# Kernel tuning notes

Hardware: AMD Instinct MI355X
Metric: run time of the kernel (lower is better)

The kernel has to match this reference:

```python
import jax, jax.numpy as jnp
import numpy as np

EPS = 1e-5
B, S, P = 2, 512, 4096
TD, SD, H, ED = 512, 384, 8, 32
HD = TD // H


def _ln(x, g, b):
    m = jnp.mean(x, axis=-1, keepdims=True)
    v = jnp.var(x, axis=-1, keepdims=True)
    return (x - m) * jax.lax.rsqrt(v + EPS) * g + b


def setup_inputs() -> dict:
    key = jax.random.key(0)
    ks = iter(jax.random.split(key, 24))

    def lin(din, dout):
        W = jax.random.normal(next(ks), (din, dout), jnp.float32) / np.sqrt(din)
        b = jnp.zeros((dout,), jnp.float32)
        return W, b

    Wq, bq = lin(TD, TD)
    Wk, bk = lin(SD, TD)
    Wv, bv = lin(SD, TD)
    Wo, bo = lin(TD, TD)
    W1, b1 = lin(TD, 4 * TD)
    W2, b2 = lin(4 * TD, TD)
    edge_emb = jax.random.normal(next(ks), (H, ED), jnp.float32)
    ep_w = jax.random.normal(next(ks), (ED,), jnp.float32) / np.sqrt(ED)
    ep_b = jnp.zeros((), jnp.float32)

    return dict(
        text_features=jax.random.normal(next(ks), (B, S, TD), jnp.float32),
        shape_features=jax.random.normal(next(ks), (B, P, SD), jnp.float32),
        tn_g=jnp.ones((TD,), jnp.float32), tn_b=jnp.zeros((TD,), jnp.float32),
        sn_g=jnp.ones((SD,), jnp.float32), sn_b=jnp.zeros((SD,), jnp.float32),
        Wq=Wq, bq=bq, Wk=Wk, bk=bk, Wv=Wv, bv=bv,
        edge_emb=edge_emb, ep_w=ep_w, ep_b=ep_b,
        Wo=Wo, bo=bo,
        on_g=jnp.ones((TD,), jnp.float32), on_b=jnp.zeros((TD,), jnp.float32),
        W1=W1, b1=b1, W2=W2, b2=b2,
        fn_g=jnp.ones((TD,), jnp.float32), fn_b=jnp.zeros((TD,), jnp.float32),
    )


def reference(text_features, shape_features, tn_g, tn_b, sn_g, sn_b,
              Wq, bq, Wk, bk, Wv, bv, edge_emb, ep_w, ep_b, Wo, bo,
              on_g, on_b, W1, b1, W2, b2, fn_g, fn_b):
    b, n, _ = text_features.shape
    tn = _ln(text_features, tn_g, tn_b)
    sn = _ln(shape_features, sn_g, sn_b)
    residual = text_features

    # [b, h, n, d] projections
    q = (tn @ Wq + bq).reshape(b, n, H, HD).transpose(0, 2, 1, 3)
    k = (sn @ Wk + bk).reshape(b, -1, H, HD).transpose(0, 2, 1, 3)
    v = (sn @ Wv + bv).reshape(b, -1, H, HD).transpose(0, 2, 1, 3)

    scale = HD ** -0.5
    base_attn = jnp.einsum('bhid,bhjd->bhij', q, k) * scale  # [b,h,n,p]

    # edge_attn[:,h] = base_attn[:,h,:,:,None] * edge_emb[h]; then Linear(ED,1)+LeakyReLU.
    # Algebraically: score = leaky_relu(base_attn * (edge_emb @ ep_w) + ep_b)
    s = edge_emb @ ep_w  # [H] per-head scalar
    edge_scores = jax.nn.leaky_relu(base_attn * s[None, :, None, None] + ep_b, 0.2)

    attn = jax.nn.softmax(base_attn + edge_scores, axis=-1)
    out = jnp.einsum('bhij,bhjd->bhid', attn, v)
    out = out.transpose(0, 2, 1, 3).reshape(b, n, TD)
    out = out @ Wo + bo
    out = _ln(residual + out, on_g, on_b)

    ffn = jax.nn.gelu(out @ W1 + b1, approximate=False) @ W2 + b2
    out = _ln(out + ffn, fn_g, fn_b)
    return out, attn
```

## Files before the change

### kernel.cpp

```cpp
#include <hip/hip_runtime.h>
#include <math.h>

#define B_  2
#define S_  512
#define P_  4096
#define TD_ 512
#define SD_ 384
#define H_  8
#define HD_ 64
#define FF_ 2048

typedef _Float16 half8 __attribute__((ext_vector_type(8)));
typedef _Float16 half4 __attribute__((ext_vector_type(4)));
typedef float floatx4 __attribute__((ext_vector_type(4)));

__device__ __forceinline__ float2 block_sum2(float a, float b) {
    for (int off = 32; off > 0; off >>= 1) {
        a += __shfl_down(a, off);
        b += __shfl_down(b, off);
    }
    __shared__ float sa[8], sb[8];
    int w = threadIdx.x >> 6;
    if ((threadIdx.x & 63) == 0) { sa[w] = a; sb[w] = b; }
    __syncthreads();
    int nw = blockDim.x >> 6;
    float ta = 0.f, tb = 0.f;
    for (int i = 0; i < nw; ++i) { ta += sa[i]; tb += sb[i]; }
    __syncthreads();
    return make_float2(ta, tb);
}

__global__ __launch_bounds__(256) void prep_kernel(
    const float* __restrict__ s0p, const float* __restrict__ s1p,
    const float* __restrict__ s2p, const float* __restrict__ s3p,
    const float* __restrict__ s4p, const float* __restrict__ s5p,
    _Float16* __restrict__ d0p, _Float16* __restrict__ d1p,
    _Float16* __restrict__ d2p, _Float16* __restrict__ d3p,
    _Float16* __restrict__ d4p, _Float16* __restrict__ d5p,
    const float* __restrict__ text, const float* __restrict__ shape,
    const float* __restrict__ tn_g, const float* __restrict__ tn_b,
    const float* __restrict__ sn_g, const float* __restrict__ sn_b,
    _Float16* __restrict__ tn_h, _Float16* __restrict__ sn_h)
{
    __shared__ float ts[32][33];
    int id = blockIdx.x;
    int tid = threadIdx.x;
    if (id < 2944) {
        const float* src; _Float16* dst; int K, N, t, nlog;
        if (id < 256)       { src=s0p; dst=d0p; K=512;  N=512;  t=id;       nlog=4; }
        else if (id < 448)  { src=s1p; dst=d1p; K=384;  N=512;  t=id-256;   nlog=4; }
        else if (id < 640)  { src=s2p; dst=d2p; K=384;  N=512;  t=id-448;   nlog=4; }
        else if (id < 896)  { src=s3p; dst=d3p; K=512;  N=512;  t=id-640;   nlog=4; }
        else if (id < 1920) { src=s4p; dst=d4p; K=512;  N=2048; t=id-896;   nlog=6; }
        else                { src=s5p; dst=d5p; K=2048; N=512;  t=id-1920;  nlog=4; }
        int n0 = (t & ((1 << nlog) - 1)) << 5;
        int k0 = (t >> nlog) << 5;
#pragma unroll
        for (int i = 0; i < 4; ++i) {
            int e = i * 256 + tid;
            int kk = e >> 5, nn = e & 31;
            ts[kk][nn] = src[(size_t)(k0 + kk) * N + n0 + nn];
        }
        __syncthreads();
#pragma unroll
        for (int i = 0; i < 4; ++i) {
            int e = i * 256 + tid;
            int nn = e >> 5, kk = e & 31;
            dst[(size_t)(n0 + nn) * K + k0 + kk] = (_Float16)ts[kk][nn];
        }
        return;
    }
    int row = id - 2944;
    const float* xr; const float* g; const float* be; _Float16* yr; int D;
    if (row < 1024) {
        D = 512; xr = text + (size_t)row * 512; g = tn_g; be = tn_b;
        yr = tn_h + (size_t)row * 512;
    } else {
        int r2 = row - 1024;
        D = 384; xr = shape + (size_t)r2 * 384; g = sn_g; be = sn_b;
        yr = sn_h + (size_t)r2 * 384;
    }
    float s = 0.f, s2 = 0.f;
    for (int i = tid; i < D; i += 256) {
        float v = xr[i]; s += v; s2 += v * v;
    }
    float2 r = block_sum2(s, s2);
    float mean = r.x / (float)D;
    float var  = r.y / (float)D - mean * mean;
    float rstd = rsqrtf(var + 1e-5f);
    for (int i = tid; i < D; i += 256)
        yr[i] = (_Float16)((xr[i] - mean) * rstd * g[i] + be[i]);
}

__global__ __launch_bounds__(256) void ln_add_kernel(
    const float* __restrict__ a, const float* __restrict__ c, int np, int cstride,
    const float* __restrict__ g, const float* __restrict__ be,
    float* __restrict__ yf, _Float16* __restrict__ yh)
{
    int row = blockIdx.x;
    int i0 = threadIdx.x, i1 = threadIdx.x + 256;
    const float* ar = a + (size_t)row * 512;
    const float* cr = c + (size_t)row * 512;
    float v0 = ar[i0], v1 = ar[i1];
    for (int t = 0; t < np; ++t) {
        v0 += cr[(size_t)t * cstride + i0];
        v1 += cr[(size_t)t * cstride + i1];
    }
    float2 rd = block_sum2(v0 + v1, v0 * v0 + v1 * v1);
    float mean = rd.x / 512.f;
    float var  = rd.y / 512.f - mean * mean;
    float rstd = rsqrtf(var + 1e-5f);
    float o0 = (v0 - mean) * rstd * g[i0] + be[i0];
    float o1 = (v1 - mean) * rstd * g[i1] + be[i1];
    if (yf) { yf[(size_t)row * 512 + i0] = o0; yf[(size_t)row * 512 + i1] = o1; }
    if (yh) { yh[(size_t)row * 512 + i0] = (_Float16)o0; yh[(size_t)row * 512 + i1] = (_Float16)o1; }
}

template<int ACT, int OUTF, int OUTH, int SPLITK>
__global__ __launch_bounds__(256) void gemm_f16_kernel(
    const _Float16* __restrict__ A, const _Float16* __restrict__ Bt,
    const float* __restrict__ bias, float* __restrict__ Cf,
    _Float16* __restrict__ Ch, int M, int N, int K)
{
    __shared__ _Float16 As[128 * 40];
    __shared__ _Float16 Bs[128 * 40];
    int tid = threadIdx.x;
    int bm = blockIdx.y * 128, bn = blockIdx.x * 128;
    int wave = tid >> 6, lane = tid & 63, quad = lane >> 4, r = lane & 15;
    int mh = (wave & 1) * 64, nh = (wave >> 1) * 64;

    floatx4 acc[4][4];
    floatx4 zz = {0.f, 0.f, 0.f, 0.f};
#pragma unroll
    for (int i = 0; i < 4; ++i)
#pragma unroll
        for (int j = 0; j < 4; ++j) acc[i][j] = zz;

    int srow = tid >> 2;
    int sko  = (tid & 3) * 8;

    int ksplit = (SPLITK > 1) ? blockIdx.z : 0;
    int kbeg = ksplit * (K / SPLITK);
    int kend = kbeg + K / SPLITK;

    const _Float16* Ap0 = A  + (size_t)(bm + srow) * K + sko;
    const _Float16* Ap1 = A  + (size_t)(bm + srow + 64) * K + sko;
    const _Float16* Bp0 = Bt + (size_t)(bn + srow) * K + sko;
    const _Float16* Bp1 = Bt + (size_t)(bn + srow + 64) * K + sko;

    half8 ra0 = *(const half8*)(Ap0 + kbeg);
    half8 ra1 = *(const half8*)(Ap1 + kbeg);
    half8 rb0 = *(const half8*)(Bp0 + kbeg);
    half8 rb1 = *(const half8*)(Bp1 + kbeg);

    for (int k0 = kbeg; k0 < kend; k0 += 32) {
        *(half8*)&As[srow * 40 + sko]        = ra0;
        *(half8*)&As[(srow + 64) * 40 + sko] = ra1;
        *(half8*)&Bs[srow * 40 + sko]        = rb0;
        *(half8*)&Bs[(srow + 64) * 40 + sko] = rb1;
        __syncthreads();
        if (k0 + 32 < kend) {
            ra0 = *(const half8*)(Ap0 + k0 + 32);
            ra1 = *(const half8*)(Ap1 + k0 + 32);
            rb0 = *(const half8*)(Bp0 + k0 + 32);
            rb1 = *(const half8*)(Bp1 + k0 + 32);
        }
        half8 af[4], bf[4];
#pragma unroll
        for (int t = 0; t < 4; ++t) {
            af[t] = *(const half8*)&As[(mh + t * 16 + r) * 40 + quad * 8];
            bf[t] = *(const half8*)&Bs[(nh + t * 16 + r) * 40 + quad * 8];
        }
#pragma unroll
        for (int i = 0; i < 4; ++i)
#pragma unroll
            for (int j = 0; j < 4; ++j)
                acc[i][j] = __builtin_amdgcn_mfma_f32_16x16x32_f16(af[i], bf[j], acc[i][j], 0, 0, 0);
        __syncthreads();
    }

#pragma unroll
    for (int j = 0; j < 4; ++j) {
        int col = bn + nh + j * 16 + r;
        float bv = (SPLITK == 1 || ksplit == 0) ? bias[col] : 0.f;
#pragma unroll
        for (int i = 0; i < 4; ++i) {
#pragma unroll
            for (int g = 0; g < 4; ++g) {
                int row = bm + mh + i * 16 + quad * 4 + g;
                float v = acc[i][j][g] + bv;
                if (ACT) v = 0.5f * v * (1.0f + erff(v * 0.70710678118654752f));
                if (OUTF) Cf[(size_t)ksplit * M * N + (size_t)row * N + col] = v;
                if (OUTH) Ch[(size_t)row * N + col] = (_Float16)v;
            }
        }
    }
}

__global__ __launch_bounds__(256) void qkv_gemm_kernel(
    const _Float16* __restrict__ tn, const _Float16* __restrict__ sn,
    const _Float16* __restrict__ Wqt, const _Float16* __restrict__ Wkt,
    const _Float16* __restrict__ Wvt,
    const float* __restrict__ bq, const float* __restrict__ bk,
    const float* __restrict__ bv,
    _Float16* __restrict__ Qh, _Float16* __restrict__ Kh, _Float16* __restrict__ Vth)
{
    __shared__ _Float16 As[128 * 40];
    __shared__ _Float16 Bs[128 * 40];
    int by = blockIdx.y;
    const _Float16* A; const _Float16* Bt; const float* bias; _Float16* out;
    int K, bm, vt;
    if (by < 8)       { A = tn; Bt = Wqt; bias = bq; K = 512; bm = by * 128;        vt = 0; out = Qh;  }
    else if (by < 72) { A = sn; Bt = Wkt; bias = bk; K = 384; bm = (by - 8) * 128;  vt = 0; out = Kh;  }
    else              { A = sn; Bt = Wvt; bias = bv; K = 384; bm = (by - 72) * 128; vt = 1; out = Vth; }
    int bn = blockIdx.x * 128;
    int tid = threadIdx.x;
    int wave = tid >> 6, lane = tid & 63, quad = lane >> 4, r = lane & 15;
    int mh = (wave & 1) * 64, nh = (wave >> 1) * 64;

    floatx4 acc[4][4];
    floatx4 zz = {0.f, 0.f, 0.f, 0.f};
#pragma unroll
    for (int i = 0; i < 4; ++i)
#pragma unroll
        for (int j = 0; j < 4; ++j) acc[i][j] = zz;

    int srow = tid >> 2;
    int sko  = (tid & 3) * 8;

    const _Float16* Ap0 = A  + (size_t)(bm + srow) * K + sko;
    const _Float16* Ap1 = A  + (size_t)(bm + srow + 64) * K + sko;
    const _Float16* Bp0 = Bt + (size_t)(bn + srow) * K + sko;
    const _Float16* Bp1 = Bt + (size_t)(bn + srow + 64) * K + sko;

    half8 ra0 = *(const half8*)(Ap0);
    half8 ra1 = *(const half8*)(Ap1);
    half8 rb0 = *(const half8*)(Bp0);
    half8 rb1 = *(const half8*)(Bp1);

    for (int k0 = 0; k0 < K; k0 += 32) {
        *(half8*)&As[srow * 40 + sko]        = ra0;
        *(half8*)&As[(srow + 64) * 40 + sko] = ra1;
        *(half8*)&Bs[srow * 40 + sko]        = rb0;
        *(half8*)&Bs[(srow + 64) * 40 + sko] = rb1;
        __syncthreads();
        if (k0 + 32 < K) {
            ra0 = *(const half8*)(Ap0 + k0 + 32);
            ra1 = *(const half8*)(Ap1 + k0 + 32);
            rb0 = *(const half8*)(Bp0 + k0 + 32);
            rb1 = *(const half8*)(Bp1 + k0 + 32);
        }
        half8 af[4], bf[4];
#pragma unroll
        for (int t = 0; t < 4; ++t) {
            af[t] = *(const half8*)&As[(mh + t * 16 + r) * 40 + quad * 8];
            bf[t] = *(const half8*)&Bs[(nh + t * 16 + r) * 40 + quad * 8];
        }
#pragma unroll
        for (int i = 0; i < 4; ++i)
#pragma unroll
            for (int j = 0; j < 4; ++j)
                acc[i][j] = __builtin_amdgcn_mfma_f32_16x16x32_f16(af[i], bf[j], acc[i][j], 0, 0, 0);
        __syncthreads();
    }

#pragma unroll
    for (int j = 0; j < 4; ++j) {
        int col = bn + nh + j * 16 + r;
        float bvv = bias[col];
#pragma unroll
        for (int i = 0; i < 4; ++i) {
#pragma unroll
            for (int g = 0; g < 4; ++g) {
                int row = bm + mh + i * 16 + quad * 4 + g;
                float v = acc[i][j][g] + bvv;
                if (!vt) {
                    out[(size_t)row * 512 + col] = (_Float16)v;
                } else {
                    int bb = row >> 12, pp = row & 4095;
                    int hh = col >> 6,  dd = col & 63;
                    out[((size_t)((bb * 8 + hh) * 64 + dd)) * 4096 + pp] = (_Float16)v;
                }
            }
        }
    }
}

__global__ __launch_bounds__(256) void score_stats_kernel(
    const _Float16* __restrict__ Qh, const _Float16* __restrict__ Kh,
    const float* __restrict__ edge_emb, const float* __restrict__ ep_w,
    const float* __restrict__ ep_b, float2* __restrict__ part)
{
    __shared__ _Float16 Qs[128 * 72];
    __shared__ _Float16 Ks[128 * 72];
    __shared__ float mred[2][128];
    __shared__ float sred[2][128];
    int p0 = blockIdx.x * 128, s0 = blockIdx.y * 128;
    int bh = blockIdx.z, h = bh & 7, b = bh >> 3;
    int tid = threadIdx.x;
    int wave = tid >> 6, lane = tid & 63, quad = lane >> 4, r = lane & 15;
    int mh = (wave & 1) * 64, nh = (wave >> 1) * 64;

#pragma unroll
    for (int i = 0; i < 4; ++i) {
        int row = i * 32 + (tid >> 3);
        int ko  = (tid & 7) * 8;
        *(half8*)&Qs[row * 72 + ko] = *(const half8*)(Qh + (size_t)(b * S_ + s0 + row) * TD_ + h * HD_ + ko);
        *(half8*)&Ks[row * 72 + ko] = *(const half8*)(Kh + (size_t)(b * P_ + p0 + row) * TD_ + h * HD_ + ko);
    }
    float s_h = 0.f;
#pragma unroll
    for (int e = 0; e < 32; ++e) s_h += edge_emb[h * 32 + e] * ep_w[e];
    float epbv = ep_b[0];
    __syncthreads();

    floatx4 acc[4][4];
    floatx4 zz = {0.f, 0.f, 0.f, 0.f};
#pragma unroll
    for (int i = 0; i < 4; ++i)
#pragma unroll
        for (int j = 0; j < 4; ++j) acc[i][j] = zz;

#pragma unroll
    for (int c = 0; c < 2; ++c) {
        half8 af[4], bf[4];
#pragma unroll
        for (int t = 0; t < 4; ++t) {
            af[t] = *(const half8*)&Qs[(mh + t * 16 + r) * 72 + c * 32 + quad * 8];
            bf[t] = *(const half8*)&Ks[(nh + t * 16 + r) * 72 + c * 32 + quad * 8];
        }
#pragma unroll
        for (int i = 0; i < 4; ++i)
#pragma unroll
            for (int j = 0; j < 4; ++j)
                acc[i][j] = __builtin_amdgcn_mfma_f32_16x16x32_f16(af[i], bf[j], acc[i][j], 0, 0, 0);
    }

    const float scale = 0.125f;
#pragma unroll
    for (int i = 0; i < 4; ++i)
#pragma unroll
        for (int j = 0; j < 4; ++j)
#pragma unroll
            for (int g = 0; g < 4; ++g) {
                float base = acc[i][j][g] * scale;
                float t = fmaf(base, s_h, epbv);
                float e = (t >= 0.f) ? t : 0.2f * t;
                acc[i][j][g] = base + e;
            }

    float mv[16], sv[16];
#pragma unroll
    for (int i = 0; i < 4; ++i)
#pragma unroll
        for (int g = 0; g < 4; ++g)
            mv[i * 4 + g] = fmaxf(fmaxf(acc[i][0][g], acc[i][1][g]),
                                  fmaxf(acc[i][2][g], acc[i][3][g]));
#pragma unroll
    for (int mask = 1; mask <= 8; mask <<= 1)
#pragma unroll
        for (int t = 0; t < 16; ++t)
            mv[t] = fmaxf(mv[t], __shfl_xor(mv[t], mask));
#pragma unroll
    for (int i = 0; i < 4; ++i)
#pragma unroll
        for (int g = 0; g < 4; ++g) {
            float s = 0.f;
#pragma unroll
            for (int j = 0; j < 4; ++j) s += __expf(acc[i][j][g] - mv[i * 4 + g]);
            sv[i * 4 + g] = s;
        }
#pragma unroll
    for (int mask = 1; mask <= 8; mask <<= 1)
#pragma unroll
        for (int t = 0; t < 16; ++t)
            sv[t] += __shfl_xor(sv[t], mask);

    if (r == 0) {
#pragma unroll
        for (int i = 0; i < 4; ++i)
#pragma unroll
            for (int g = 0; g < 4; ++g) {
                int row = mh + i * 16 + quad * 4 + g;
                mred[wave >> 1][row] = mv[i * 4 + g];
                sred[wave >> 1][row] = sv[i * 4 + g];
            }
    }
    __syncthreads();
    if (tid < 128) {
        float m0 = mred[0][tid], m1 = mred[1][tid];
        float m = fmaxf(m0, m1);
        float s = sred[0][tid] * __expf(m0 - m) + sred[1][tid] * __expf(m1 - m);
        part[(size_t)blockIdx.x * (B_ * H_ * S_) + (size_t)bh * S_ + s0 + tid] = make_float2(m, s);
    }
}

__global__ __launch_bounds__(256) void attn_pv_kernel(
    const _Float16* __restrict__ Qh, const _Float16* __restrict__ Kh,
    const _Float16* __restrict__ Vt,
    const float* __restrict__ edge_emb, const float* __restrict__ ep_w,
    const float* __restrict__ ep_b, const float2* __restrict__ part,
    float* __restrict__ attn, float* __restrict__ ctx_part)
{
    __shared__ _Float16 Qs[32 * 72];
    __shared__ _Float16 Ks[128 * 72];
    __shared__ _Float16 Vs[64 * 136];
    __shared__ _Float16 As[32 * 136];
    __shared__ float2 ms_sh[32];

    int s0 = blockIdx.x * 32;
    int split = blockIdx.y;
    int bh = blockIdx.z, h = bh & 7, b = bh >> 3;
    int tid = threadIdx.x;
    int wave = tid >> 6, lane = tid & 63, quad = lane >> 4, r = lane & 15;

    {
        int row = tid >> 3, ko = (tid & 7) * 8;
        *(half8*)&Qs[row * 72 + ko] =
            *(const half8*)(Qh + (size_t)(b * S_ + s0 + row) * TD_ + h * HD_ + ko);
    }
    if (tid < 32) {
        int base = bh * S_ + s0 + tid;
        float2 v = part[base];
        float m = v.x, l = v.y;
#pragma unroll
        for (int t = 1; t < 32; ++t) {
            float2 p = part[(size_t)t * (B_ * H_ * S_) + base];
            float nm = fmaxf(m, p.x);
            l = l * __expf(m - nm) + p.y * __expf(p.x - nm);
            m = nm;
        }
        ms_sh[tid] = make_float2(m, 1.0f / l);
    }

    float s_h = 0.f;
#pragma unroll
    for (int e = 0; e < 32; ++e) s_h += edge_emb[h * 32 + e] * ep_w[e];
    float epbv = ep_b[0];

    const _Float16* Kbase = Kh + (size_t)b * P_ * TD_ + h * HD_;
    const _Float16* Vbase = Vt + (size_t)bh * 64 * P_;

    int pg0 = split * 512;
    half8 rk[4], rv[4];
#pragma unroll
    for (int ii = 0; ii < 4; ++ii) {
        int e = ii * 256 + tid;
        rk[ii] = *(const half8*)(Kbase + (size_t)(pg0 + (e >> 3)) * TD_ + (e & 7) * 8);
        rv[ii] = *(const half8*)(Vbase + (size_t)(e >> 4) * P_ + pg0 + (e & 15) * 8);
    }

    floatx4 zz = {0.f, 0.f, 0.f, 0.f};
    floatx4 accpv[2];
    accpv[0] = zz; accpv[1] = zz;
    const float scale = 0.125f;

    for (int c = 0; c < 4; ++c) {
        int pg = pg0 + c * 128;
#pragma unroll
        for (int ii = 0; ii < 4; ++ii) {
            int e = ii * 256 + tid;
            *(half8*)&Ks[(e >> 3) * 72 + (e & 7) * 8]  = rk[ii];
            *(half8*)&Vs[(e >> 4) * 136 + (e & 15) * 8] = rv[ii];
        }
        __syncthreads();
        if (c < 3) {
            int pn = pg + 128;
#pragma unroll
            for (int ii = 0; ii < 4; ++ii) {
                int e = ii * 256 + tid;
                rk[ii] = *(const half8*)(Kbase + (size_t)(pn + (e >> 3)) * TD_ + (e & 7) * 8);
                rv[ii] = *(const half8*)(Vbase + (size_t)(e >> 4) * P_ + pn + (e & 15) * 8);
            }
        }

        floatx4 accs[2][2];
        accs[0][0] = zz; accs[0][1] = zz; accs[1][0] = zz; accs[1][1] = zz;
#pragma unroll
        for (int c2 = 0; c2 < 2; ++c2) {
            half8 aq[2], bk2[2];
#pragma unroll
            for (int i = 0; i < 2; ++i)
                aq[i] = *(const half8*)&Qs[(i * 16 + r) * 72 + c2 * 32 + quad * 8];
#pragma unroll
            for (int j = 0; j < 2; ++j)
                bk2[j] = *(const half8*)&Ks[(wave * 32 + j * 16 + r) * 72 + c2 * 32 + quad * 8];
#pragma unroll
            for (int i = 0; i < 2; ++i)
#pragma unroll
                for (int j = 0; j < 2; ++j)
                    accs[i][j] = __builtin_amdgcn_mfma_f32_16x16x32_f16(aq[i], bk2[j], accs[i][j], 0, 0, 0);
        }

#pragma unroll
        for (int i = 0; i < 2; ++i)
#pragma unroll
            for (int j = 0; j < 2; ++j) {
                int colp = wave * 32 + j * 16 + r;
#pragma unroll
                for (int g = 0; g < 4; ++g) {
                    int srow = i * 16 + quad * 4 + g;
                    float base = accs[i][j][g] * scale;
                    float t = fmaf(base, s_h, epbv);
                    float e = (t >= 0.f) ? t : 0.2f * t;
                    float z = base + e;
                    float2 ms = ms_sh[srow];
                    float p = __expf(z - ms.x) * ms.y;
                    __builtin_nontemporal_store(p, &attn[((size_t)bh * S_ + s0 + srow) * P_ + pg + colp]);
                    As[srow * 136 + colp] = (_Float16)p;
                }
            }
        __syncthreads();

#pragma unroll
        for (int cc = 0; cc < 4; ++cc) {
            half8 bv = *(const half8*)&Vs[(wave * 16 + r) * 136 + cc * 32 + quad * 8];
#pragma unroll
            for (int i2 = 0; i2 < 2; ++i2) {
                half8 ap = *(const half8*)&As[(i2 * 16 + r) * 136 + cc * 32 + quad * 8];
                accpv[i2] = __builtin_amdgcn_mfma_f32_16x16x32_f16(ap, bv, accpv[i2], 0, 0, 0);
            }
        }
        __syncthreads();
    }

    float* dst = ctx_part + (size_t)split * (1024 * 512);
#pragma unroll
    for (int i2 = 0; i2 < 2; ++i2)
#pragma unroll
        for (int g = 0; g < 4; ++g) {
            int srow = s0 + i2 * 16 + quad * 4 + g;
            int d = wave * 16 + r;
            dst[(size_t)(b * S_ + srow) * TD_ + h * HD_ + d] = accpv[i2][g];
        }
}

__global__ __launch_bounds__(256) void sumcast_kernel(
    const float4* __restrict__ src, _Float16* __restrict__ dst, int n4)
{
    int i = blockIdx.x * 256 + threadIdx.x;
    if (i < n4) {
        float4 v = src[i];
#pragma unroll
        for (int t = 1; t < 8; ++t) {
            float4 p = src[i + t * 131072];
            v.x += p.x; v.y += p.y; v.z += p.z; v.w += p.w;
        }
        half4 hv = { (_Float16)v.x, (_Float16)v.y, (_Float16)v.z, (_Float16)v.w };
        *(half4*)&dst[(size_t)i * 4] = hv;
    }
}

extern "C" void kernel_launch(void* const* d_in, const int* in_sizes, int n_in,
                              void* d_out, int out_size, void* d_ws, size_t ws_size,
                              hipStream_t stream) {
    const float* text  = (const float*)d_in[0];
    const float* shape = (const float*)d_in[1];
    const float* tn_g  = (const float*)d_in[2];
    const float* tn_b  = (const float*)d_in[3];
    const float* sn_g  = (const float*)d_in[4];
    const float* sn_b  = (const float*)d_in[5];
    const float* Wq    = (const float*)d_in[6];
    const float* bq    = (const float*)d_in[7];
    const float* Wk    = (const float*)d_in[8];
    const float* bk    = (const float*)d_in[9];
    const float* Wv    = (const float*)d_in[10];
    const float* bv    = (const float*)d_in[11];
    const float* edge  = (const float*)d_in[12];
    const float* epw   = (const float*)d_in[13];
    const float* epb   = (const float*)d_in[14];
    const float* Wo    = (const float*)d_in[15];
    const float* bo    = (const float*)d_in[16];
    const float* on_g  = (const float*)d_in[17];
    const float* on_b  = (const float*)d_in[18];
    const float* W1    = (const float*)d_in[19];
    const float* b1    = (const float*)d_in[20];
    const float* W2    = (const float*)d_in[21];
    const float* b2    = (const float*)d_in[22];
    const float* fn_g  = (const float*)d_in[23];
    const float* fn_b  = (const float*)d_in[24];

    float* out_f  = (float*)d_out;
    float* attn_f = out_f + (size_t)B_ * S_ * TD_;

    char* w = (char*)d_ws;
    _Float16* tn_h   = (_Float16*)w; w += (size_t)1024 * 512 * 2;
    _Float16* sn_h   = (_Float16*)w; w += (size_t)8192 * 384 * 2;
    _Float16* Q_h    = (_Float16*)w; w += (size_t)1024 * 512 * 2;
    _Float16* K_h    = (_Float16*)w; w += (size_t)8192 * 512 * 2;
    _Float16* Vt_h   = (_Float16*)w; w += (size_t)16 * 64 * 4096 * 2;
    _Float16* ctx_h  = (_Float16*)w; w += (size_t)1024 * 512 * 2;
    _Float16* out1_h = (_Float16*)w; w += (size_t)1024 * 512 * 2;
    _Float16* h1_h   = (_Float16*)w; w += (size_t)1024 * 2048 * 2;
    _Float16* Wqt    = (_Float16*)w; w += (size_t)512 * 512 * 2;
    _Float16* Wkt    = (_Float16*)w; w += (size_t)512 * 384 * 2;
    _Float16* Wvt    = (_Float16*)w; w += (size_t)512 * 384 * 2;
    _Float16* Wot    = (_Float16*)w; w += (size_t)512 * 512 * 2;
    _Float16* W1t    = (_Float16*)w; w += (size_t)2048 * 512 * 2;
    _Float16* W2t    = (_Float16*)w; w += (size_t)512 * 2048 * 2;
    float*    out1_f = (float*)w;    w += (size_t)1024 * 512 * 4;
    float*    ctx_part = (float*)w;  w += (size_t)8 * 1024 * 512 * 4;

    float2* part = (float2*)sn_h;

    prep_kernel<<<2944 + 1024 + 8192, 256, 0, stream>>>(
        Wq, Wk, Wv, Wo, W1, W2, Wqt, Wkt, Wvt, Wot, W1t, W2t,
        text, shape, tn_g, tn_b, sn_g, sn_b, tn_h, sn_h);

    qkv_gemm_kernel<<<dim3(4, 136), 256, 0, stream>>>(tn_h, sn_h, Wqt, Wkt, Wvt,
                                                      bq, bk, bv, Q_h, K_h, Vt_h);

    score_stats_kernel<<<dim3(P_ / 128, S_ / 128, B_ * H_), 256, 0, stream>>>(
        Q_h, K_h, edge, epw, epb, part);
    attn_pv_kernel<<<dim3(S_ / 32, 8, B_ * H_), 256, 0, stream>>>(
        Q_h, K_h, Vt_h, edge, epw, epb, part, attn_f, ctx_part);
    sumcast_kernel<<<dim3(512), 256, 0, stream>>>((const float4*)ctx_part, ctx_h, 131072);

    gemm_f16_kernel<0,1,0,4><<<dim3(4, 8, 4), 256, 0, stream>>>(ctx_h, Wot, bo, ctx_part, nullptr, 1024, 512, 512);
    ln_add_kernel<<<B_ * S_, 256, 0, stream>>>(text, ctx_part, 4, 1024 * 512, on_g, on_b, out1_f, out1_h);

    gemm_f16_kernel<1,0,1,1><<<dim3(16, 8), 256, 0, stream>>>(out1_h, W1t, b1, nullptr, h1_h, 1024, 2048, 512);
    gemm_f16_kernel<0,1,0,4><<<dim3(4, 8, 4), 256, 0, stream>>>(h1_h, W2t, b2, ctx_part, nullptr, 1024, 512, 2048);
    ln_add_kernel<<<B_ * S_, 256, 0, stream>>>(out1_f, ctx_part, 4, 1024 * 512, fn_g, fn_b, out_f, nullptr);
}
```

Before: 356.2 us.

## Fuse softmax stats and PV into single two-pass attention kernel; enlarge QKV tiles

Replaces the separate score-statistics kernel, the split-P attention/PV kernel and the ctx sum-cast kernel with one kernel per (32-query block, head). It makes two passes over all of P: the first builds the running max and sum, the second writes normalized probabilities and accumulates PV directly into fp16 ctx. This removes the partial-stat buffer, the 8-way ctx partials and the reduction kernel. In exchange the grid shrinks to 256 blocks that each loop over 4096 keys twice, which cuts parallelism and recomputes QK^T. The QKV GEMM also moves to 512-thread blocks with 256-row A tiles.

New measurement: 391.1 us. +9.8%, slower.

```diff
diff --git a/kernel.cpp b/kernel.cpp
--- a/kernel.cpp
+++ b/kernel.cpp
@@ -197,7 +197,7 @@
     }
 }
 
-__global__ __launch_bounds__(256) void qkv_gemm_kernel(
+__global__ __launch_bounds__(512) void qkv_gemm_kernel(
     const _Float16* __restrict__ tn, const _Float16* __restrict__ sn,
     const _Float16* __restrict__ Wqt, const _Float16* __restrict__ Wkt,
     const _Float16* __restrict__ Wvt,
@@ -205,18 +205,18 @@
     const float* __restrict__ bv,
     _Float16* __restrict__ Qh, _Float16* __restrict__ Kh, _Float16* __restrict__ Vth)
 {
-    __shared__ _Float16 As[128 * 40];
+    __shared__ _Float16 As[256 * 40];
     __shared__ _Float16 Bs[128 * 40];
     int by = blockIdx.y;
     const _Float16* A; const _Float16* Bt; const float* bias; _Float16* out;
     int K, bm, vt;
-    if (by < 8)       { A = tn; Bt = Wqt; bias = bq; K = 512; bm = by * 128;        vt = 0; out = Qh;  }
-    else if (by < 72) { A = sn; Bt = Wkt; bias = bk; K = 384; bm = (by - 8) * 128;  vt = 0; out = Kh;  }
-    else              { A = sn; Bt = Wvt; bias = bv; K = 384; bm = (by - 72) * 128; vt = 1; out = Vth; }
+    if (by < 4)       { A = tn; Bt = Wqt; bias = bq; K = 512; bm = by * 256;        vt = 0; out = Qh;  }
+    else if (by < 36) { A = sn; Bt = Wkt; bias = bk; K = 384; bm = (by - 4) * 256;  vt = 0; out = Kh;  }
+    else              { A = sn; Bt = Wvt; bias = bv; K = 384; bm = (by - 36) * 256; vt = 1; out = Vth; }
     int bn = blockIdx.x * 128;
     int tid = threadIdx.x;
     int wave = tid >> 6, lane = tid & 63, quad = lane >> 4, r = lane & 15;
-    int mh = (wave & 1) * 64, nh = (wave >> 1) * 64;
+    int mh = (wave >> 1) * 64, nh = (wave & 1) * 64;
 
     floatx4 acc[4][4];
     floatx4 zz = {0.f, 0.f, 0.f, 0.f};
@@ -225,30 +225,24 @@
 #pragma unroll
         for (int j = 0; j < 4; ++j) acc[i][j] = zz;
 
-    int srow = tid >> 2;
-    int sko  = (tid & 3) * 8;
-
-    const _Float16* Ap0 = A  + (size_t)(bm + srow) * K + sko;
-    const _Float16* Ap1 = A  + (size_t)(bm + srow + 64) * K + sko;
-    const _Float16* Bp0 = Bt + (size_t)(bn + srow) * K + sko;
-    const _Float16* Bp1 = Bt + (size_t)(bn + srow + 64) * K + sko;
-
-    half8 ra0 = *(const half8*)(Ap0);
-    half8 ra1 = *(const half8*)(Ap1);
-    half8 rb0 = *(const half8*)(Bp0);
-    half8 rb1 = *(const half8*)(Bp1);
+    int arow = tid >> 2, ako = (tid & 3) * 8;
+    const _Float16* ApA0 = A  + (size_t)(bm + arow) * K + ako;
+    const _Float16* ApA1 = A  + (size_t)(bm + arow + 128) * K + ako;
+    const _Float16* BpB  = Bt + (size_t)(bn + arow) * K + ako;
+
+    half8 ra0 = *(const half8*)(ApA0);
+    half8 ra1 = *(const half8*)(ApA1);
+    half8 rb  = *(const half8*)(BpB);
 
     for (int k0 = 0; k0 < K; k0 += 32) {
-        *(half8*)&As[srow * 40 + sko]        = ra0;
-        *(half8*)&As[(srow + 64) * 40 + sko] = ra1;
-        *(half8*)&Bs[srow * 40 + sko]        = rb0;
-        *(half8*)&Bs[(srow + 64) * 40 + sko] = rb1;
+        *(half8*)&As[arow * 40 + ako]         = ra0;
+        *(half8*)&As[(arow + 128) * 40 + ako] = ra1;
+        *(half8*)&Bs[arow * 40 + ako]         = rb;
         __syncthreads();
         if (k0 + 32 < K) {
-            ra0 = *(const half8*)(Ap0 + k0 + 32);
-            ra1 = *(const half8*)(Ap1 + k0 + 32);
-            rb0 = *(const half8*)(Bp0 + k0 + 32);
-            rb1 = *(const half8*)(Bp1 + k0 + 32);
+            ra0 = *(const half8*)(ApA0 + k0 + 32);
+            ra1 = *(const half8*)(ApA1 + k0 + 32);
+            rb  = *(const half8*)(BpB  + k0 + 32);
         }
         half8 af[4], bf[4];
 #pragma unroll
@@ -286,268 +280,176 @@
     }
 }
 
-__global__ __launch_bounds__(256) void score_stats_kernel(
-    const _Float16* __restrict__ Qh, const _Float16* __restrict__ Kh,
-    const float* __restrict__ edge_emb, const float* __restrict__ ep_w,
-    const float* __restrict__ ep_b, float2* __restrict__ part)
-{
-    __shared__ _Float16 Qs[128 * 72];
-    __shared__ _Float16 Ks[128 * 72];
-    __shared__ float mred[2][128];
-    __shared__ float sred[2][128];
-    int p0 = blockIdx.x * 128, s0 = blockIdx.y * 128;
-    int bh = blockIdx.z, h = bh & 7, b = bh >> 3;
-    int tid = threadIdx.x;
-    int wave = tid >> 6, lane = tid & 63, quad = lane >> 4, r = lane & 15;
-    int mh = (wave & 1) * 64, nh = (wave >> 1) * 64;
-
-#pragma unroll
-    for (int i = 0; i < 4; ++i) {
-        int row = i * 32 + (tid >> 3);
-        int ko  = (tid & 7) * 8;
-        *(half8*)&Qs[row * 72 + ko] = *(const half8*)(Qh + (size_t)(b * S_ + s0 + row) * TD_ + h * HD_ + ko);
-        *(half8*)&Ks[row * 72 + ko] = *(const half8*)(Kh + (size_t)(b * P_ + p0 + row) * TD_ + h * HD_ + ko);
-    }
-    float s_h = 0.f;
-#pragma unroll
-    for (int e = 0; e < 32; ++e) s_h += edge_emb[h * 32 + e] * ep_w[e];
-    float epbv = ep_b[0];
-    __syncthreads();
-
-    floatx4 acc[4][4];
-    floatx4 zz = {0.f, 0.f, 0.f, 0.f};
-#pragma unroll
-    for (int i = 0; i < 4; ++i)
-#pragma unroll
-        for (int j = 0; j < 4; ++j) acc[i][j] = zz;
-
-#pragma unroll
-    for (int c = 0; c < 2; ++c) {
-        half8 af[4], bf[4];
-#pragma unroll
-        for (int t = 0; t < 4; ++t) {
-            af[t] = *(const half8*)&Qs[(mh + t * 16 + r) * 72 + c * 32 + quad * 8];
-            bf[t] = *(const half8*)&Ks[(nh + t * 16 + r) * 72 + c * 32 + quad * 8];
-        }
-#pragma unroll
-        for (int i = 0; i < 4; ++i)
-#pragma unroll
-            for (int j = 0; j < 4; ++j)
-                acc[i][j] = __builtin_amdgcn_mfma_f32_16x16x32_f16(af[i], bf[j], acc[i][j], 0, 0, 0);
-    }
-
-    const float scale = 0.125f;
-#pragma unroll
-    for (int i = 0; i < 4; ++i)
-#pragma unroll
-        for (int j = 0; j < 4; ++j)
-#pragma unroll
-            for (int g = 0; g < 4; ++g) {
-                float base = acc[i][j][g] * scale;
-                float t = fmaf(base, s_h, epbv);
-                float e = (t >= 0.f) ? t : 0.2f * t;
-                acc[i][j][g] = base + e;
-            }
-
-    float mv[16], sv[16];
-#pragma unroll
-    for (int i = 0; i < 4; ++i)
-#pragma unroll
-        for (int g = 0; g < 4; ++g)
-            mv[i * 4 + g] = fmaxf(fmaxf(acc[i][0][g], acc[i][1][g]),
-                                  fmaxf(acc[i][2][g], acc[i][3][g]));
-#pragma unroll
-    for (int mask = 1; mask <= 8; mask <<= 1)
-#pragma unroll
-        for (int t = 0; t < 16; ++t)
-            mv[t] = fmaxf(mv[t], __shfl_xor(mv[t], mask));
-#pragma unroll
-    for (int i = 0; i < 4; ++i)
-#pragma unroll
-        for (int g = 0; g < 4; ++g) {
-            float s = 0.f;
-#pragma unroll
-            for (int j = 0; j < 4; ++j) s += __expf(acc[i][j][g] - mv[i * 4 + g]);
-            sv[i * 4 + g] = s;
-        }
-#pragma unroll
-    for (int mask = 1; mask <= 8; mask <<= 1)
-#pragma unroll
-        for (int t = 0; t < 16; ++t)
-            sv[t] += __shfl_xor(sv[t], mask);
-
-    if (r == 0) {
-#pragma unroll
-        for (int i = 0; i < 4; ++i)
-#pragma unroll
-            for (int g = 0; g < 4; ++g) {
-                int row = mh + i * 16 + quad * 4 + g;
-                mred[wave >> 1][row] = mv[i * 4 + g];
-                sred[wave >> 1][row] = sv[i * 4 + g];
-            }
-    }
-    __syncthreads();
-    if (tid < 128) {
-        float m0 = mred[0][tid], m1 = mred[1][tid];
-        float m = fmaxf(m0, m1);
-        float s = sred[0][tid] * __expf(m0 - m) + sred[1][tid] * __expf(m1 - m);
-        part[(size_t)blockIdx.x * (B_ * H_ * S_) + (size_t)bh * S_ + s0 + tid] = make_float2(m, s);
-    }
-}
-
-__global__ __launch_bounds__(256) void attn_pv_kernel(
+__global__ __launch_bounds__(512) void flash_attn_kernel(
     const _Float16* __restrict__ Qh, const _Float16* __restrict__ Kh,
     const _Float16* __restrict__ Vt,
     const float* __restrict__ edge_emb, const float* __restrict__ ep_w,
-    const float* __restrict__ ep_b, const float2* __restrict__ part,
-    float* __restrict__ attn, float* __restrict__ ctx_part)
+    const float* __restrict__ ep_b,
+    float* __restrict__ attn, _Float16* __restrict__ ctx_h)
 {
     __shared__ _Float16 Qs[32 * 72];
     __shared__ _Float16 Ks[128 * 72];
     __shared__ _Float16 Vs[64 * 136];
     __shared__ _Float16 As[32 * 136];
-    __shared__ float2 ms_sh[32];
+    __shared__ float cm[8][32], cl[8][32];
 
     int s0 = blockIdx.x * 32;
-    int split = blockIdx.y;
-    int bh = blockIdx.z, h = bh & 7, b = bh >> 3;
+    int bh = blockIdx.y, h = bh & 7, b = bh >> 3;
     int tid = threadIdx.x;
     int wave = tid >> 6, lane = tid & 63, quad = lane >> 4, r = lane & 15;
-
-    {
+    int sH = wave >> 2, pQ = wave & 3;
+
+    if (tid < 256) {
         int row = tid >> 3, ko = (tid & 7) * 8;
         *(half8*)&Qs[row * 72 + ko] =
             *(const half8*)(Qh + (size_t)(b * S_ + s0 + row) * TD_ + h * HD_ + ko);
     }
-    if (tid < 32) {
-        int base = bh * S_ + s0 + tid;
-        float2 v = part[base];
-        float m = v.x, l = v.y;
-#pragma unroll
-        for (int t = 1; t < 32; ++t) {
-            float2 p = part[(size_t)t * (B_ * H_ * S_) + base];
-            float nm = fmaxf(m, p.x);
-            l = l * __expf(m - nm) + p.y * __expf(p.x - nm);
-            m = nm;
-        }
-        ms_sh[tid] = make_float2(m, 1.0f / l);
-    }
-
     float s_h = 0.f;
 #pragma unroll
     for (int e = 0; e < 32; ++e) s_h += edge_emb[h * 32 + e] * ep_w[e];
     float epbv = ep_b[0];
+    const float scale = 0.125f;
 
     const _Float16* Kbase = Kh + (size_t)b * P_ * TD_ + h * HD_;
     const _Float16* Vbase = Vt + (size_t)bh * 64 * P_;
 
-    int pg0 = split * 512;
-    half8 rk[4], rv[4];
-#pragma unroll
-    for (int ii = 0; ii < 4; ++ii) {
-        int e = ii * 256 + tid;
-        rk[ii] = *(const half8*)(Kbase + (size_t)(pg0 + (e >> 3)) * TD_ + (e & 7) * 8);
-        rv[ii] = *(const half8*)(Vbase + (size_t)(e >> 4) * P_ + pg0 + (e & 15) * 8);
-    }
+    int krow = tid >> 3, kko = (tid & 7) * 8;
+    int vrow = tid >> 4, vpo = (tid & 15) * 8;
 
     floatx4 zz = {0.f, 0.f, 0.f, 0.f};
-    floatx4 accpv[2];
-    accpv[0] = zz; accpv[1] = zz;
-    const float scale = 0.125f;
-
-    for (int c = 0; c < 4; ++c) {
-        int pg = pg0 + c * 128;
-#pragma unroll
-        for (int ii = 0; ii < 4; ++ii) {
-            int e = ii * 256 + tid;
-            *(half8*)&Ks[(e >> 3) * 72 + (e & 7) * 8]  = rk[ii];
-            *(half8*)&Vs[(e >> 4) * 136 + (e & 15) * 8] = rv[ii];
-        }
-        __syncthreads();
-        if (c < 3) {
-            int pn = pg + 128;
-#pragma unroll
-            for (int ii = 0; ii < 4; ++ii) {
-                int e = ii * 256 + tid;
-                rk[ii] = *(const half8*)(Kbase + (size_t)(pn + (e >> 3)) * TD_ + (e & 7) * 8);
-                rv[ii] = *(const half8*)(Vbase + (size_t)(e >> 4) * P_ + pn + (e & 15) * 8);
-            }
-        }
-
-        floatx4 accs[2][2];
-        accs[0][0] = zz; accs[0][1] = zz; accs[1][0] = zz; accs[1][1] = zz;
+    float m_run[4], l_run[4];
+#pragma unroll
+    for (int g = 0; g < 4; ++g) { m_run[g] = -1e30f; l_run[g] = 0.f; }
+
+    half8 rk0 = *(const half8*)(Kbase + (size_t)krow * TD_ + kko);
+    half8 rk1 = *(const half8*)(Kbase + (size_t)(krow + 64) * TD_ + kko);
+
+    for (int pc = 0; pc < P_; pc += 128) {
+        *(half8*)&Ks[krow * 72 + kko]        = rk0;
+        *(half8*)&Ks[(krow + 64) * 72 + kko] = rk1;
+        __syncthreads();
+        if (pc + 128 < P_) {
+            rk0 = *(const half8*)(Kbase + (size_t)(pc + 128 + krow) * TD_ + kko);
+            rk1 = *(const half8*)(Kbase + (size_t)(pc + 128 + krow + 64) * TD_ + kko);
+        }
+        floatx4 accs[2];
+        accs[0] = zz; accs[1] = zz;
 #pragma unroll
         for (int c2 = 0; c2 < 2; ++c2) {
-            half8 aq[2], bk2[2];
-#pragma unroll
-            for (int i = 0; i < 2; ++i)
-                aq[i] = *(const half8*)&Qs[(i * 16 + r) * 72 + c2 * 32 + quad * 8];
-#pragma unroll
-            for (int j = 0; j < 2; ++j)
-                bk2[j] = *(const half8*)&Ks[(wave * 32 + j * 16 + r) * 72 + c2 * 32 + quad * 8];
-#pragma unroll
-            for (int i = 0; i < 2; ++i)
-#pragma unroll
-                for (int j = 0; j < 2; ++j)
-                    accs[i][j] = __builtin_amdgcn_mfma_f32_16x16x32_f16(aq[i], bk2[j], accs[i][j], 0, 0, 0);
-        }
-
-#pragma unroll
-        for (int i = 0; i < 2; ++i)
+            half8 aq = *(const half8*)&Qs[(sH * 16 + r) * 72 + c2 * 32 + quad * 8];
 #pragma unroll
             for (int j = 0; j < 2; ++j) {
-                int colp = wave * 32 + j * 16 + r;
-#pragma unroll
-                for (int g = 0; g < 4; ++g) {
-                    int srow = i * 16 + quad * 4 + g;
-                    float base = accs[i][j][g] * scale;
-                    float t = fmaf(base, s_h, epbv);
-                    float e = (t >= 0.f) ? t : 0.2f * t;
-                    float z = base + e;
-                    float2 ms = ms_sh[srow];
-                    float p = __expf(z - ms.x) * ms.y;
-                    __builtin_nontemporal_store(p, &attn[((size_t)bh * S_ + s0 + srow) * P_ + pg + colp]);
-                    As[srow * 136 + colp] = (_Float16)p;
-                }
-            }
-        __syncthreads();
-
+                half8 bk = *(const half8*)&Ks[(pQ * 32 + j * 16 + r) * 72 + c2 * 32 + quad * 8];
+                accs[j] = __builtin_amdgcn_mfma_f32_16x16x32_f16(aq, bk, accs[j], 0, 0, 0);
+            }
+        }
+        float zv[2][4];
+#pragma unroll
+        for (int j = 0; j < 2; ++j)
+#pragma unroll
+            for (int g = 0; g < 4; ++g) {
+                float base = accs[j][g] * scale;
+                float t = fmaf(base, s_h, epbv);
+                float e = (t >= 0.f) ? t : 0.2f * t;
+                zv[j][g] = base + e;
+            }
+        float mw[4], sw[4];
+#pragma unroll
+        for (int g = 0; g < 4; ++g) {
+            mw[g] = fmaxf(zv[0][g], zv[1][g]);
+#pragma unroll
+            for (int mask = 1; mask <= 8; mask <<= 1)
+                mw[g] = fmaxf(mw[g], __shfl_xor(mw[g], mask));
+            sw[g] = __expf(zv[0][g] - mw[g]) + __expf(zv[1][g] - mw[g]);
+#pragma unroll
+            for (int mask = 1; mask <= 8; mask <<= 1)
+                sw[g] += __shfl_xor(sw[g], mask);
+        }
+        if (r == 0) {
+#pragma unroll
+            for (int g = 0; g < 4; ++g) {
+                cm[wave][sH * 16 + quad * 4 + g] = mw[g];
+                cl[wave][sH * 16 + quad * 4 + g] = sw[g];
+            }
+        }
+        __syncthreads();
+#pragma unroll
+        for (int g = 0; g < 4; ++g) {
+            int row = sH * 16 + quad * 4 + g;
+#pragma unroll
+            for (int q2 = 0; q2 < 4; ++q2) {
+                float mc = cm[sH * 4 + q2][row];
+                float lc = cl[sH * 4 + q2][row];
+                float nm = fmaxf(m_run[g], mc);
+                l_run[g] = l_run[g] * __expf(m_run[g] - nm) + lc * __expf(mc - nm);
+                m_run[g] = nm;
+            }
+        }
+    }
+    float invl[4];
+#pragma unroll
+    for (int g = 0; g < 4; ++g) invl[g] = 1.0f / l_run[g];
+
+    half8 prk0 = *(const half8*)(Kbase + (size_t)krow * TD_ + kko);
+    half8 prk1 = *(const half8*)(Kbase + (size_t)(krow + 64) * TD_ + kko);
+    half8 prv0 = *(const half8*)(Vbase + (size_t)vrow * P_ + vpo);
+    half8 prv1 = *(const half8*)(Vbase + (size_t)(vrow + 32) * P_ + vpo);
+
+    floatx4 accpv = zz;
+
+    for (int pc = 0; pc < P_; pc += 128) {
+        *(half8*)&Ks[krow * 72 + kko]         = prk0;
+        *(half8*)&Ks[(krow + 64) * 72 + kko]  = prk1;
+        *(half8*)&Vs[vrow * 136 + vpo]        = prv0;
+        *(half8*)&Vs[(vrow + 32) * 136 + vpo] = prv1;
+        __syncthreads();
+        if (pc + 128 < P_) {
+            prk0 = *(const half8*)(Kbase + (size_t)(pc + 128 + krow) * TD_ + kko);
+            prk1 = *(const half8*)(Kbase + (size_t)(pc + 128 + krow + 64) * TD_ + kko);
+            prv0 = *(const half8*)(Vbase + (size_t)vrow * P_ + pc + 128 + vpo);
+            prv1 = *(const half8*)(Vbase + (size_t)(vrow + 32) * P_ + pc + 128 + vpo);
+        }
+        floatx4 accs[2];
+        accs[0] = zz; accs[1] = zz;
+#pragma unroll
+        for (int c2 = 0; c2 < 2; ++c2) {
+            half8 aq = *(const half8*)&Qs[(sH * 16 + r) * 72 + c2 * 32 + quad * 8];
+#pragma unroll
+            for (int j = 0; j < 2; ++j) {
+                half8 bk = *(const half8*)&Ks[(pQ * 32 + j * 16 + r) * 72 + c2 * 32 + quad * 8];
+                accs[j] = __builtin_amdgcn_mfma_f32_16x16x32_f16(aq, bk, accs[j], 0, 0, 0);
+            }
+        }
+#pragma unroll
+        for (int j = 0; j < 2; ++j) {
+            int colp = pQ * 32 + j * 16 + r;
+#pragma unroll
+            for (int g = 0; g < 4; ++g) {
+                int srow = sH * 16 + quad * 4 + g;
+                float base = accs[j][g] * scale;
+                float t = fmaf(base, s_h, epbv);
+                float e = (t >= 0.f) ? t : 0.2f * t;
+                float z = base + e;
+                float p = __expf(z - m_run[g]) * invl[g];
+                __builtin_nontemporal_store(p, &attn[((size_t)bh * S_ + s0 + srow) * P_ + pc + colp]);
+                As[srow * 136 + colp] = (_Float16)p;
+            }
+        }
+        __syncthreads();
 #pragma unroll
         for (int cc = 0; cc < 4; ++cc) {
-            half8 bv = *(const half8*)&Vs[(wave * 16 + r) * 136 + cc * 32 + quad * 8];
-#pragma unroll
-            for (int i2 = 0; i2 < 2; ++i2) {
-                half8 ap = *(const half8*)&As[(i2 * 16 + r) * 136 + cc * 32 + quad * 8];
-                accpv[i2] = __builtin_amdgcn_mfma_f32_16x16x32_f16(ap, bv, accpv[i2], 0, 0, 0);
-            }
-        }
-        __syncthreads();
-    }
-
-    float* dst = ctx_part + (size_t)split * (1024 * 512);
-#pragma unroll
-    for (int i2 = 0; i2 < 2; ++i2)
-#pragma unroll
-        for (int g = 0; g < 4; ++g) {
-            int srow = s0 + i2 * 16 + quad * 4 + g;
-            int d = wave * 16 + r;
-            dst[(size_t)(b * S_ + srow) * TD_ + h * HD_ + d] = accpv[i2][g];
-        }
-}
-
-__global__ __launch_bounds__(256) void sumcast_kernel(
-    const float4* __restrict__ src, _Float16* __restrict__ dst, int n4)
-{
-    int i = blockIdx.x * 256 + threadIdx.x;
-    if (i < n4) {
-        float4 v = src[i];
-#pragma unroll
-        for (int t = 1; t < 8; ++t) {
-            float4 p = src[i + t * 131072];
-            v.x += p.x; v.y += p.y; v.z += p.z; v.w += p.w;
-        }
-        half4 hv = { (_Float16)v.x, (_Float16)v.y, (_Float16)v.z, (_Float16)v.w };
-        *(half4*)&dst[(size_t)i * 4] = hv;
+            half8 bv = *(const half8*)&Vs[(pQ * 16 + r) * 136 + cc * 32 + quad * 8];
+            half8 ap = *(const half8*)&As[(sH * 16 + r) * 136 + cc * 32 + quad * 8];
+            accpv = __builtin_amdgcn_mfma_f32_16x16x32_f16(ap, bv, accpv, 0, 0, 0);
+        }
+        __syncthreads();
+    }
+
+#pragma unroll
+    for (int g = 0; g < 4; ++g) {
+        int srow = s0 + sH * 16 + quad * 4 + g;
+        int d = pQ * 16 + r;
+        ctx_h[(size_t)(b * S_ + srow) * TD_ + h * HD_ + d] = (_Float16)accpv[g];
     }
 }
 
@@ -599,22 +501,17 @@
     _Float16* W1t    = (_Float16*)w; w += (size_t)2048 * 512 * 2;
     _Float16* W2t    = (_Float16*)w; w += (size_t)512 * 2048 * 2;
     float*    out1_f = (float*)w;    w += (size_t)1024 * 512 * 4;
-    float*    ctx_part = (float*)w;  w += (size_t)8 * 1024 * 512 * 4;
-
-    float2* part = (float2*)sn_h;
+    float*    ctx_part = (float*)w;  w += (size_t)4 * 1024 * 512 * 4;
 
     prep_kernel<<<2944 + 1024 + 8192, 256, 0, stream>>>(
         Wq, Wk, Wv, Wo, W1, W2, Wqt, Wkt, Wvt, Wot, W1t, W2t,
         text, shape, tn_g, tn_b, sn_g, sn_b, tn_h, sn_h);
 
-    qkv_gemm_kernel<<<dim3(4, 136), 256, 0, stream>>>(tn_h, sn_h, Wqt, Wkt, Wvt,
-                                                      bq, bk, bv, Q_h, K_h, Vt_h);
-
-    score_stats_kernel<<<dim3(P_ / 128, S_ / 128, B_ * H_), 256, 0, stream>>>(
-        Q_h, K_h, edge, epw, epb, part);
-    attn_pv_kernel<<<dim3(S_ / 32, 8, B_ * H_), 256, 0, stream>>>(
-        Q_h, K_h, Vt_h, edge, epw, epb, part, attn_f, ctx_part);
-    sumcast_kernel<<<dim3(512), 256, 0, stream>>>((const float4*)ctx_part, ctx_h, 131072);
+    qkv_gemm_kernel<<<dim3(4, 68), 512, 0, stream>>>(tn_h, sn_h, Wqt, Wkt, Wvt,
+                                                     bq, bk, bv, Q_h, K_h, Vt_h);
+
+    flash_attn_kernel<<<dim3(S_ / 32, B_ * H_), 512, 0, stream>>>(
+        Q_h, K_h, Vt_h, edge, epw, epb, attn_f, ctx_h);
 
     gemm_f16_kernel<0,1,0,4><<<dim3(4, 8, 4), 256, 0, stream>>>(ctx_h, Wot, bo, ctx_part, nullptr, 1024, 512, 512);
     ln_add_kernel<<<B_ * S_, 256, 0, stream>>>(text, ctx_part, 4, 1024 * 512, on_g, on_b, out1_f, out1_h);
```
